# Kernel tuning notes

Measured on AMD Instinct MI355X. Metric: run time of the kernel, lower is better.

Reference implementation:

```python
import jax, jax.numpy as jnp
import numpy as np

N = 2048
IN_C, HID, LAT = 128, 128, 64
E_SPARSE = 65536


def gcn_conv(x, W, b, src, dst, w, n):
    # PyG GCNConv: h = D^-1/2 (A+I) D^-1/2 (x W) + b  (self-loops already in edge list)
    deg = jax.ops.segment_sum(w, dst, num_segments=n)
    dinv = jnp.where(deg > 0, jax.lax.rsqrt(deg), 0.0)
    norm = dinv[src] * w * dinv[dst]            # [E]
    h = x @ W                                   # [N, out]
    agg = jax.ops.segment_sum(h[src] * norm[:, None], dst, num_segments=n)
    return agg + b


def setup_inputs() -> dict:
    key = jax.random.key(0)
    ks = jax.random.split(key, 9)
    x = jax.random.normal(ks[0], (N, IN_C), jnp.float32)
    masked_y = jax.random.normal(ks[1], (N, N), jnp.float32)
    edge_index = jax.random.randint(ks[2], (2, E_SPARSE), 0, N, dtype=jnp.int32)
    s = 0.05
    W1 = jax.random.normal(ks[3], (IN_C, HID), jnp.float32) * s
    b1 = jnp.zeros((HID,), jnp.float32)
    Wmu = jax.random.normal(ks[4], (HID, LAT), jnp.float32) * s
    bmu = jnp.zeros((LAT,), jnp.float32)
    Wls = jax.random.normal(ks[5], (HID, LAT), jnp.float32) * s
    bls = jnp.zeros((LAT,), jnp.float32)
    return {"x": x, "masked_y": masked_y, "W1": W1, "b1": b1,
            "Wmu": Wmu, "bmu": bmu, "Wls": Wls, "bls": bls,
            "edge_index": edge_index}


def reference(x, masked_y, W1, b1, Wmu, bmu, Wls, bls, edge_index):
    n = x.shape[0]
    half = n // 2
    # masking leaves only the top-left [half, half] block of masked_y nonzero;
    # dense_to_sparse on that block -> all half*half (row, col) pairs (entries != 0 a.s.)
    rows = jnp.repeat(jnp.arange(half, dtype=edge_index.dtype), half)
    cols = jnp.tile(jnp.arange(half, dtype=edge_index.dtype), half)
    y_w = jax.nn.sigmoid(masked_y[:half, :half].reshape(-1))
    loop = jnp.arange(n, dtype=edge_index.dtype)
    src = jnp.concatenate([edge_index[0], rows, loop])
    dst = jnp.concatenate([edge_index[1], cols, loop])
    w = jnp.concatenate([jnp.ones((edge_index.shape[1],), x.dtype), y_w,
                         jnp.ones((n,), x.dtype)])
    hidden = jax.nn.relu(gcn_conv(x, W1, b1, src, dst, w, n))
    z_mu = gcn_conv(hidden, Wmu, bmu, src, dst, w, n)
    z_logstd = gcn_conv(hidden, Wls, bls, src, dst, w, n)
    return (z_mu, z_logstd)
```

## Files before the change

### kernel.cpp

```cpp
#include <hip/hip_runtime.h>

#define NN 2048
#define HALF 1024
#define CC 128
#define EE 65536
#define CAP 128

typedef unsigned short u16;

__device__ __forceinline__ float sigm(float v){ return 1.0f/(1.0f + __expf(-v)); }

__device__ __forceinline__ float dinv_lo(int i, const int* __restrict__ cnt,
                                         const float* __restrict__ colsum){
  return rsqrtf(1.0f + (float)cnt[i] + colsum[i]);
}
__device__ __forceinline__ float dinv_any(int i, const int* __restrict__ cnt,
                                          const float* __restrict__ colsum){
  float cs = (i < HALF) ? colsum[i] : 0.0f;
  return rsqrtf(1.0f + (float)cnt[i] + cs);
}

__global__ __launch_bounds__(256) void k_prep(
    const float* __restrict__ my, const int* __restrict__ ei, const float* __restrict__ x,
    const float* __restrict__ W1,
    const float* __restrict__ bmu, const float* __restrict__ bls,
    float* __restrict__ SpRaw, float* __restrict__ colsum,
    int* __restrict__ cnt, u16* __restrict__ bucket, float* __restrict__ H0,
    float* __restrict__ out)
{
  __shared__ float la[8][CC];
  int b = blockIdx.x, t = threadIdx.x;
  int gid = b*256 + t;
  if (gid < 65536) {
    int g4 = (gid & 15)*4;
    const float* bb = (gid < 32768) ? bmu : bls;
    ((float4*)out)[gid] = make_float4(bb[g4], bb[g4+1], bb[g4+2], bb[g4+3]);
  }

  if (b < 128) {
    int c0 = t*4;
    float cs0=0.f, cs1=0.f, cs2=0.f, cs3=0.f;
    #pragma unroll 2
    for (int rr=0; rr<8; ++rr){
      int r = b*8 + rr;
      float4 v = *(const float4*)(my + (size_t)r*NN + c0);
      float s0=sigm(v.x), s1=sigm(v.y), s2=sigm(v.z), s3=sigm(v.w);
      *(float4*)(SpRaw + (size_t)r*HALF + c0) = make_float4(s0,s1,s2,s3);
      cs0+=s0; cs1+=s1; cs2+=s2; cs3+=s3;
    }
    atomicAdd(&colsum[c0+0], cs0);
    atomicAdd(&colsum[c0+1], cs1);
    atomicAdd(&colsum[c0+2], cs2);
    atomicAdd(&colsum[c0+3], cs3);
  } else if (b < 256) {
    int e0 = (b-128)*512 + t;
    #pragma unroll
    for (int i=0;i<2;i++){
      int e = e0 + i*256;
      int s = ei[e], d = ei[EE + e];
      int slot = atomicAdd(&cnt[d], 1);
      if (slot < CAP) bucket[d*CAP + slot] = (u16)s;
    }
  } else {
    int row0 = (b-256)*8;
    #pragma unroll
    for (int i=0;i<4;i++){
      int idx = i*256 + t;
      la[idx>>7][idx&127] = x[(size_t)row0*CC + idx];
    }
    __syncthreads();
    int f = t & 127, rh = t >> 7;
    const float4* a0 = (const float4*)la[rh*4+0];
    const float4* a1 = (const float4*)la[rh*4+1];
    const float4* a2 = (const float4*)la[rh*4+2];
    const float4* a3 = (const float4*)la[rh*4+3];
    float o0=0.f, o1=0.f, o2=0.f, o3=0.f;
    #pragma unroll 4
    for (int k4=0;k4<32;k4++){
      float4 v0=a0[k4], v1=a1[k4], v2=a2[k4], v3=a3[k4];
      float w0 = W1[(k4*4+0)*CC + f];
      float w1 = W1[(k4*4+1)*CC + f];
      float w2 = W1[(k4*4+2)*CC + f];
      float w3 = W1[(k4*4+3)*CC + f];
      o0=fmaf(v0.x,w0,o0); o0=fmaf(v0.y,w1,o0); o0=fmaf(v0.z,w2,o0); o0=fmaf(v0.w,w3,o0);
      o1=fmaf(v1.x,w0,o1); o1=fmaf(v1.y,w1,o1); o1=fmaf(v1.z,w2,o1); o1=fmaf(v1.w,w3,o1);
      o2=fmaf(v2.x,w0,o2); o2=fmaf(v2.y,w1,o2); o2=fmaf(v2.z,w2,o2); o2=fmaf(v2.w,w3,o2);
      o3=fmaf(v3.x,w0,o3); o3=fmaf(v3.y,w1,o3); o3=fmaf(v3.z,w2,o3); o3=fmaf(v3.w,w3,o3);
    }
    H0[(size_t)(row0 + rh*4 + 0)*CC + f] = o0;
    H0[(size_t)(row0 + rh*4 + 1)*CC + f] = o1;
    H0[(size_t)(row0 + rh*4 + 2)*CC + f] = o2;
    H0[(size_t)(row0 + rh*4 + 3)*CC + f] = o3;
  }
}

__global__ __launch_bounds__(256) void k_layer1(
  const float* __restrict__ SpRaw, const float* __restrict__ H0,
  const int* __restrict__ cnt, const float* __restrict__ colsum,
  const u16* __restrict__ bucket,
  float* __restrict__ SP, float* __restrict__ DP)
{
  int b = blockIdx.x, t = threadIdx.x;
  if (b < 512) {
    __shared__ float srow[128];
    int chunk = b & 7, r0 = chunk*128;
    if (t < 128) srow[t] = dinv_lo(r0 + t, cnt, colsum);
    __syncthreads();
    int lane = t & 63, f0 = lane*2;
    int dbase = (b>>3)*16 + (t>>6)*4;
    float a00=0.f,a01=0.f,a10=0.f,a11=0.f,a20=0.f,a21=0.f,a30=0.f,a31=0.f;
    #pragma unroll 4
    for (int rr=0; rr<128; ++rr){
      int r = r0 + rr;
      float2 fv = *(const float2*)(H0 + (size_t)r*CC + f0);
      float sc = srow[rr];
      float fx = fv.x*sc, fy = fv.y*sc;
      float4 s4 = *(const float4*)(SpRaw + (size_t)r*HALF + dbase);
      a00=fmaf(s4.x,fx,a00); a01=fmaf(s4.x,fy,a01);
      a10=fmaf(s4.y,fx,a10); a11=fmaf(s4.y,fy,a11);
      a20=fmaf(s4.z,fx,a20); a21=fmaf(s4.z,fy,a21);
      a30=fmaf(s4.w,fx,a30); a31=fmaf(s4.w,fy,a31);
    }
    float d0=dinv_lo(dbase+0,cnt,colsum), d1=dinv_lo(dbase+1,cnt,colsum);
    float d2=dinv_lo(dbase+2,cnt,colsum), d3=dinv_lo(dbase+3,cnt,colsum);
    float* o = DP + ((size_t)chunk*HALF + dbase)*CC + f0;
    o[0*CC+0]=a00*d0; o[0*CC+1]=a01*d0;
    o[1*CC+0]=a10*d1; o[1*CC+1]=a11*d1;
    o[2*CC+0]=a20*d2; o[2*CC+1]=a21*d2;
    o[3*CC+0]=a30*d3; o[3*CC+1]=a31*d3;
  } else {
    __shared__ float sdinv[NN];
    #pragma unroll
    for (int i=0;i<8;i++){
      int j = i*256 + t;
      float cs = (j < HALF) ? colsum[j] : 0.0f;
      sdinv[j] = rsqrtf(1.0f + (float)cnt[j] + cs);
    }
    __syncthreads();
    int w = t>>6, hw = (t>>5)&1, l = t&31;
    int d = (b-512)*8 + w*2 + hw;
    int f0 = l*4;
    float dd = sdinv[d];
    float4 sv = *(const float4*)(H0 + (size_t)d*CC + f0);
    float ax=dd*sv.x, ay=dd*sv.y, az=dd*sv.z, aw=dd*sv.w;
    int m = cnt[d]; m = m > CAP ? CAP : m;
    const u16* bk = bucket + d*CAP;
    int j = 0;
    for (; j+1 < m; j += 2){
      unsigned pr = *(const unsigned*)(bk + j);
      int s0 = pr & 0xffff, s1 = pr >> 16;
      float w0 = sdinv[s0], w1 = sdinv[s1];
      float4 v0 = *(const float4*)(H0 + (size_t)s0*CC + f0);
      float4 v1 = *(const float4*)(H0 + (size_t)s1*CC + f0);
      ax=fmaf(w0,v0.x,ax); ay=fmaf(w0,v0.y,ay); az=fmaf(w0,v0.z,az); aw=fmaf(w0,v0.w,aw);
      ax=fmaf(w1,v1.x,ax); ay=fmaf(w1,v1.y,ay); az=fmaf(w1,v1.z,az); aw=fmaf(w1,v1.w,aw);
    }
    if (j < m){
      int s0 = bk[j];
      float w0 = sdinv[s0];
      float4 v0 = *(const float4*)(H0 + (size_t)s0*CC + f0);
      ax=fmaf(w0,v0.x,ax); ay=fmaf(w0,v0.y,ay); az=fmaf(w0,v0.z,az); aw=fmaf(w0,v0.w,aw);
    }
    *(float4*)(SP + (size_t)d*CC + f0) = make_float4(dd*ax, dd*ay, dd*az, dd*aw);
  }
}

__global__ __launch_bounds__(256) void k_mid(
  const float* __restrict__ SP, const float* __restrict__ DP,
  const float* __restrict__ b1,
  const float* __restrict__ Wmu, const float* __restrict__ Wls,
  const int* __restrict__ cnt, const float* __restrict__ colsum,
  float* __restrict__ Gm)
{
  __shared__ float la[4][CC];
  int b = blockIdx.x, t = threadIdx.x;
  int row0 = b*4;
  #pragma unroll
  for (int i=0;i<2;i++){
    int idx = i*256 + t;
    int r = row0 + (idx>>7), c = idx & 127;
    float v = SP[(size_t)r*CC + c];
    if (r < HALF){
      #pragma unroll
      for (int k=0;k<8;k++) v += DP[((size_t)k*HALF + r)*CC + c];
    }
    v += b1[c];
    la[idx>>7][c] = v > 0.f ? v : 0.f;
  }
  __syncthreads();
  int f = t & 127, rh = t >> 7, g = f & 63;
  const float* W = (f < 64) ? Wmu : Wls;
  const float4* a0 = (const float4*)la[rh*2+0];
  const float4* a1 = (const float4*)la[rh*2+1];
  float o0=0.f, o1=0.f;
  #pragma unroll 4
  for (int k4=0;k4<32;k4++){
    float4 v0=a0[k4], v1=a1[k4];
    float w0 = W[(k4*4+0)*64 + g];
    float w1 = W[(k4*4+1)*64 + g];
    float w2 = W[(k4*4+2)*64 + g];
    float w3 = W[(k4*4+3)*64 + g];
    o0=fmaf(v0.x,w0,o0); o0=fmaf(v0.y,w1,o0); o0=fmaf(v0.z,w2,o0); o0=fmaf(v0.w,w3,o0);
    o1=fmaf(v1.x,w0,o1); o1=fmaf(v1.y,w1,o1); o1=fmaf(v1.z,w2,o1); o1=fmaf(v1.w,w3,o1);
  }
  int rA = row0 + rh*2;
  Gm[(size_t)(rA+0)*CC + f] = o0 * dinv_any(rA+0, cnt, colsum);
  Gm[(size_t)(rA+1)*CC + f] = o1 * dinv_any(rA+1, cnt, colsum);
}

__global__ __launch_bounds__(256) void k_layer2(
  const float* __restrict__ SpRaw, const float* __restrict__ Gm,
  const int* __restrict__ cnt, const float* __restrict__ colsum,
  const u16* __restrict__ bucket, float* __restrict__ out)
{
  int b = blockIdx.x, t = threadIdx.x;
  if (b < 512) {
    int lane = t & 63, f0 = lane*2;
    size_t obase = (f0 < 64) ? 0 : (size_t)NN*64;
    int g0 = f0 & 63;
    int dbase = (b>>3)*16 + (t>>6)*4;
    int r0 = (b&7)*128;
    float a00=0.f,a01=0.f,a10=0.f,a11=0.f,a20=0.f,a21=0.f,a30=0.f,a31=0.f;
    #pragma unroll 4
    for (int rr=0; rr<128; ++rr){
      int r = r0 + rr;
      float2 gv = *(const float2*)(Gm + (size_t)r*CC + f0);
      float4 s4 = *(const float4*)(SpRaw + (size_t)r*HALF + dbase);
      a00=fmaf(s4.x,gv.x,a00); a01=fmaf(s4.x,gv.y,a01);
      a10=fmaf(s4.y,gv.x,a10); a11=fmaf(s4.y,gv.y,a11);
      a20=fmaf(s4.z,gv.x,a20); a21=fmaf(s4.z,gv.y,a21);
      a30=fmaf(s4.w,gv.x,a30); a31=fmaf(s4.w,gv.y,a31);
    }
    float d0=dinv_lo(dbase+0,cnt,colsum), d1=dinv_lo(dbase+1,cnt,colsum);
    float d2=dinv_lo(dbase+2,cnt,colsum), d3=dinv_lo(dbase+3,cnt,colsum);
    float* o = out + obase + (size_t)dbase*64 + g0;
    atomicAdd(o + 0*64 + 0, a00*d0); atomicAdd(o + 0*64 + 1, a01*d0);
    atomicAdd(o + 1*64 + 0, a10*d1); atomicAdd(o + 1*64 + 1, a11*d1);
    atomicAdd(o + 2*64 + 0, a20*d2); atomicAdd(o + 2*64 + 1, a21*d2);
    atomicAdd(o + 3*64 + 0, a30*d3); atomicAdd(o + 3*64 + 1, a31*d3);
  } else {
    int w = t>>6, hw = (t>>5)&1, l = t&31;
    int d = (b-512)*8 + w*2 + hw;
    int f0 = l*4;
    size_t obase = (f0 < 64) ? 0 : (size_t)NN*64;
    int g0 = f0 & 63;
    float4 a = *(const float4*)(Gm + (size_t)d*CC + f0);
    float ax=a.x, ay=a.y, az=a.z, aw=a.w;
    int m = cnt[d]; m = m > CAP ? CAP : m;
    const u16* bk = bucket + d*CAP;
    int j = 0;
    for (; j+1 < m; j += 2){
      unsigned pr = *(const unsigned*)(bk + j);
      int s0 = pr & 0xffff, s1 = pr >> 16;
      float4 v0 = *(const float4*)(Gm + (size_t)s0*CC + f0);
      float4 v1 = *(const float4*)(Gm + (size_t)s1*CC + f0);
      ax += v0.x + v1.x; ay += v0.y + v1.y;
      az += v0.z + v1.z; aw += v0.w + v1.w;
    }
    if (j < m){
      int s0 = bk[j];
      float4 v0 = *(const float4*)(Gm + (size_t)s0*CC + f0);
      ax += v0.x; ay += v0.y; az += v0.z; aw += v0.w;
    }
    float dd = dinv_any(d, cnt, colsum);
    float* o = out + obase + (size_t)d*64 + g0;
    atomicAdd(o + 0, dd*ax); atomicAdd(o + 1, dd*ay);
    atomicAdd(o + 2, dd*az); atomicAdd(o + 3, dd*aw);
  }
}

extern "C" void kernel_launch(void* const* d_in, const int* in_sizes, int n_in,
                              void* d_out, int out_size, void* d_ws, size_t ws_size,
                              hipStream_t stream)
{
  (void)in_sizes; (void)n_in; (void)out_size; (void)ws_size;
  const float* x   = (const float*)d_in[0];
  const float* my  = (const float*)d_in[1];
  const float* W1  = (const float*)d_in[2];
  const float* b1  = (const float*)d_in[3];
  const float* Wmu = (const float*)d_in[4];
  const float* bmu = (const float*)d_in[5];
  const float* Wls = (const float*)d_in[6];
  const float* bls = (const float*)d_in[7];
  const int*   ei  = (const int*)d_in[8];
  float* out = (float*)d_out;
  char* ws = (char*)d_ws;

  int*   cnt    = (int*)  (ws + 0);
  float* colsum = (float*)(ws + 8192);
  u16*   bucket = (u16*)  (ws + 12288);
  float* SpRaw  = (float*)(ws + 536576);
  float* H0     = (float*)(ws + 4730880);
  float* Gm     = (float*)(ws + 5779456);
  float* SP     = (float*)(ws + 6828032);
  float* DP     = (float*)(ws + 7876608);

  hipMemsetAsync(ws, 0, 12288, stream);
  k_prep  <<<512, 256, 0, stream>>>(my, ei, x, W1, bmu, bls,
                                    SpRaw, colsum, cnt, bucket, H0, out);
  k_layer1<<<768, 256, 0, stream>>>(SpRaw, H0, cnt, colsum, bucket, SP, DP);
  k_mid   <<<512, 256, 0, stream>>>(SP, DP, b1, Wmu, Wls, cnt, colsum, Gm);
  k_layer2<<<768, 256, 0, stream>>>(SpRaw, Gm, cnt, colsum, bucket, out);
}
```

Measured before the change: 153.9 us.

## Aggregate raw x before W1 matmul and widen dense-aggregation register tiles

```diff
diff --git a/kernel.cpp b/kernel.cpp
--- a/kernel.cpp
+++ b/kernel.cpp
@@ -21,22 +21,13 @@
 }
 
 __global__ __launch_bounds__(256) void k_prep(
-    const float* __restrict__ my, const int* __restrict__ ei, const float* __restrict__ x,
-    const float* __restrict__ W1,
+    const float* __restrict__ my, const int* __restrict__ ei,
     const float* __restrict__ bmu, const float* __restrict__ bls,
     float* __restrict__ SpRaw, float* __restrict__ colsum,
-    int* __restrict__ cnt, u16* __restrict__ bucket, float* __restrict__ H0,
+    int* __restrict__ cnt, u16* __restrict__ bucket,
     float* __restrict__ out)
 {
-  __shared__ float la[8][CC];
-  int b = blockIdx.x, t = threadIdx.x;
-  int gid = b*256 + t;
-  if (gid < 65536) {
-    int g4 = (gid & 15)*4;
-    const float* bb = (gid < 32768) ? bmu : bls;
-    ((float4*)out)[gid] = make_float4(bb[g4], bb[g4+1], bb[g4+2], bb[g4+3]);
-  }
-
+  int b = blockIdx.x, t = threadIdx.x;
   if (b < 128) {
     int c0 = t*4;
     float cs0=0.f, cs1=0.f, cs2=0.f, cs3=0.f;
@@ -52,82 +43,54 @@
     atomicAdd(&colsum[c0+1], cs1);
     atomicAdd(&colsum[c0+2], cs2);
     atomicAdd(&colsum[c0+3], cs3);
-  } else if (b < 256) {
-    int e0 = (b-128)*512 + t;
-    #pragma unroll
-    for (int i=0;i<2;i++){
-      int e = e0 + i*256;
-      int s = ei[e], d = ei[EE + e];
-      int slot = atomicAdd(&cnt[d], 1);
-      if (slot < CAP) bucket[d*CAP + slot] = (u16)s;
-    }
   } else {
-    int row0 = (b-256)*8;
-    #pragma unroll
-    for (int i=0;i<4;i++){
-      int idx = i*256 + t;
-      la[idx>>7][idx&127] = x[(size_t)row0*CC + idx];
-    }
-    __syncthreads();
-    int f = t & 127, rh = t >> 7;
-    const float4* a0 = (const float4*)la[rh*4+0];
-    const float4* a1 = (const float4*)la[rh*4+1];
-    const float4* a2 = (const float4*)la[rh*4+2];
-    const float4* a3 = (const float4*)la[rh*4+3];
-    float o0=0.f, o1=0.f, o2=0.f, o3=0.f;
-    #pragma unroll 4
-    for (int k4=0;k4<32;k4++){
-      float4 v0=a0[k4], v1=a1[k4], v2=a2[k4], v3=a3[k4];
-      float w0 = W1[(k4*4+0)*CC + f];
-      float w1 = W1[(k4*4+1)*CC + f];
-      float w2 = W1[(k4*4+2)*CC + f];
-      float w3 = W1[(k4*4+3)*CC + f];
-      o0=fmaf(v0.x,w0,o0); o0=fmaf(v0.y,w1,o0); o0=fmaf(v0.z,w2,o0); o0=fmaf(v0.w,w3,o0);
-      o1=fmaf(v1.x,w0,o1); o1=fmaf(v1.y,w1,o1); o1=fmaf(v1.z,w2,o1); o1=fmaf(v1.w,w3,o1);
-      o2=fmaf(v2.x,w0,o2); o2=fmaf(v2.y,w1,o2); o2=fmaf(v2.z,w2,o2); o2=fmaf(v2.w,w3,o2);
-      o3=fmaf(v3.x,w0,o3); o3=fmaf(v3.y,w1,o3); o3=fmaf(v3.z,w2,o3); o3=fmaf(v3.w,w3,o3);
-    }
-    H0[(size_t)(row0 + rh*4 + 0)*CC + f] = o0;
-    H0[(size_t)(row0 + rh*4 + 1)*CC + f] = o1;
-    H0[(size_t)(row0 + rh*4 + 2)*CC + f] = o2;
-    H0[(size_t)(row0 + rh*4 + 3)*CC + f] = o3;
-  }
-}
-
-__global__ __launch_bounds__(256) void k_layer1(
-  const float* __restrict__ SpRaw, const float* __restrict__ H0,
+    int bb = b - 128;
+    int gid = bb*256 + t;
+    int g4 = (gid & 15)*4;
+    const float* bbias = (gid < 32768) ? bmu : bls;
+    ((float4*)out)[gid] = make_float4(bbias[g4], bbias[g4+1], bbias[g4+2], bbias[g4+3]);
+    int e = bb*256 + t;
+    int s = ei[e], d = ei[EE + e];
+    int slot = atomicAdd(&cnt[d], 1);
+    if (slot < CAP) bucket[d*CAP + slot] = (u16)s;
+  }
+}
+
+__global__ __launch_bounds__(256) void k_agg1(
+  const float* __restrict__ SpRaw, const float* __restrict__ x,
   const int* __restrict__ cnt, const float* __restrict__ colsum,
   const u16* __restrict__ bucket,
   float* __restrict__ SP, float* __restrict__ DP)
 {
   int b = blockIdx.x, t = threadIdx.x;
-  if (b < 512) {
+  if (b < 256) {
     __shared__ float srow[128];
     int chunk = b & 7, r0 = chunk*128;
     if (t < 128) srow[t] = dinv_lo(r0 + t, cnt, colsum);
     __syncthreads();
-    int lane = t & 63, f0 = lane*2;
-    int dbase = (b>>3)*16 + (t>>6)*4;
-    float a00=0.f,a01=0.f,a10=0.f,a11=0.f,a20=0.f,a21=0.f,a30=0.f,a31=0.f;
-    #pragma unroll 4
+    int sub = t >> 5, l = t & 31;
+    int f0 = l*4;
+    int dbase = (b>>3)*32 + sub*4;
+    float4 a0 = make_float4(0.f,0.f,0.f,0.f), a1 = a0, a2 = a0, a3 = a0;
+    #pragma unroll 2
     for (int rr=0; rr<128; ++rr){
       int r = r0 + rr;
-      float2 fv = *(const float2*)(H0 + (size_t)r*CC + f0);
+      float4 xv = *(const float4*)(x + (size_t)r*CC + f0);
       float sc = srow[rr];
-      float fx = fv.x*sc, fy = fv.y*sc;
+      float x0=xv.x*sc, x1=xv.y*sc, x2=xv.z*sc, x3=xv.w*sc;
       float4 s4 = *(const float4*)(SpRaw + (size_t)r*HALF + dbase);
-      a00=fmaf(s4.x,fx,a00); a01=fmaf(s4.x,fy,a01);
-      a10=fmaf(s4.y,fx,a10); a11=fmaf(s4.y,fy,a11);
-      a20=fmaf(s4.z,fx,a20); a21=fmaf(s4.z,fy,a21);
-      a30=fmaf(s4.w,fx,a30); a31=fmaf(s4.w,fy,a31);
+      a0.x=fmaf(s4.x,x0,a0.x); a0.y=fmaf(s4.x,x1,a0.y); a0.z=fmaf(s4.x,x2,a0.z); a0.w=fmaf(s4.x,x3,a0.w);
+      a1.x=fmaf(s4.y,x0,a1.x); a1.y=fmaf(s4.y,x1,a1.y); a1.z=fmaf(s4.y,x2,a1.z); a1.w=fmaf(s4.y,x3,a1.w);
+      a2.x=fmaf(s4.z,x0,a2.x); a2.y=fmaf(s4.z,x1,a2.y); a2.z=fmaf(s4.z,x2,a2.z); a2.w=fmaf(s4.z,x3,a2.w);
+      a3.x=fmaf(s4.w,x0,a3.x); a3.y=fmaf(s4.w,x1,a3.y); a3.z=fmaf(s4.w,x2,a3.z); a3.w=fmaf(s4.w,x3,a3.w);
     }
     float d0=dinv_lo(dbase+0,cnt,colsum), d1=dinv_lo(dbase+1,cnt,colsum);
     float d2=dinv_lo(dbase+2,cnt,colsum), d3=dinv_lo(dbase+3,cnt,colsum);
     float* o = DP + ((size_t)chunk*HALF + dbase)*CC + f0;
-    o[0*CC+0]=a00*d0; o[0*CC+1]=a01*d0;
-    o[1*CC+0]=a10*d1; o[1*CC+1]=a11*d1;
-    o[2*CC+0]=a20*d2; o[2*CC+1]=a21*d2;
-    o[3*CC+0]=a30*d3; o[3*CC+1]=a31*d3;
+    *(float4*)(o + 0*CC) = make_float4(a0.x*d0, a0.y*d0, a0.z*d0, a0.w*d0);
+    *(float4*)(o + 1*CC) = make_float4(a1.x*d1, a1.y*d1, a1.z*d1, a1.w*d1);
+    *(float4*)(o + 2*CC) = make_float4(a2.x*d2, a2.y*d2, a2.z*d2, a2.w*d2);
+    *(float4*)(o + 3*CC) = make_float4(a3.x*d3, a3.y*d3, a3.z*d3, a3.w*d3);
   } else {
     __shared__ float sdinv[NN];
     #pragma unroll
@@ -138,10 +101,10 @@
     }
     __syncthreads();
     int w = t>>6, hw = (t>>5)&1, l = t&31;
-    int d = (b-512)*8 + w*2 + hw;
+    int d = (b-256)*8 + w*2 + hw;
     int f0 = l*4;
     float dd = sdinv[d];
-    float4 sv = *(const float4*)(H0 + (size_t)d*CC + f0);
+    float4 sv = *(const float4*)(x + (size_t)d*CC + f0);
     float ax=dd*sv.x, ay=dd*sv.y, az=dd*sv.z, aw=dd*sv.w;
     int m = cnt[d]; m = m > CAP ? CAP : m;
     const u16* bk = bucket + d*CAP;
@@ -150,15 +113,15 @@
       unsigned pr = *(const unsigned*)(bk + j);
       int s0 = pr & 0xffff, s1 = pr >> 16;
       float w0 = sdinv[s0], w1 = sdinv[s1];
-      float4 v0 = *(const float4*)(H0 + (size_t)s0*CC + f0);
-      float4 v1 = *(const float4*)(H0 + (size_t)s1*CC + f0);
+      float4 v0 = *(const float4*)(x + (size_t)s0*CC + f0);
+      float4 v1 = *(const float4*)(x + (size_t)s1*CC + f0);
       ax=fmaf(w0,v0.x,ax); ay=fmaf(w0,v0.y,ay); az=fmaf(w0,v0.z,az); aw=fmaf(w0,v0.w,aw);
       ax=fmaf(w1,v1.x,ax); ay=fmaf(w1,v1.y,ay); az=fmaf(w1,v1.z,az); aw=fmaf(w1,v1.w,aw);
     }
     if (j < m){
       int s0 = bk[j];
       float w0 = sdinv[s0];
-      float4 v0 = *(const float4*)(H0 + (size_t)s0*CC + f0);
+      float4 v0 = *(const float4*)(x + (size_t)s0*CC + f0);
       ax=fmaf(w0,v0.x,ax); ay=fmaf(w0,v0.y,ay); az=fmaf(w0,v0.z,az); aw=fmaf(w0,v0.w,aw);
     }
     *(float4*)(SP + (size_t)d*CC + f0) = make_float4(dd*ax, dd*ay, dd*az, dd*aw);
@@ -167,12 +130,13 @@
 
 __global__ __launch_bounds__(256) void k_mid(
   const float* __restrict__ SP, const float* __restrict__ DP,
-  const float* __restrict__ b1,
+  const float* __restrict__ b1, const float* __restrict__ W1,
   const float* __restrict__ Wmu, const float* __restrict__ Wls,
   const int* __restrict__ cnt, const float* __restrict__ colsum,
   float* __restrict__ Gm)
 {
   __shared__ float la[4][CC];
+  __shared__ float lb[4][CC];
   int b = blockIdx.x, t = threadIdx.x;
   int row0 = b*4;
   #pragma unroll
@@ -184,63 +148,90 @@
       #pragma unroll
       for (int k=0;k<8;k++) v += DP[((size_t)k*HALF + r)*CC + c];
     }
-    v += b1[c];
-    la[idx>>7][c] = v > 0.f ? v : 0.f;
+    la[idx>>7][c] = v;
   }
   __syncthreads();
-  int f = t & 127, rh = t >> 7, g = f & 63;
-  const float* W = (f < 64) ? Wmu : Wls;
-  const float4* a0 = (const float4*)la[rh*2+0];
-  const float4* a1 = (const float4*)la[rh*2+1];
-  float o0=0.f, o1=0.f;
-  #pragma unroll 4
-  for (int k4=0;k4<32;k4++){
-    float4 v0=a0[k4], v1=a1[k4];
-    float w0 = W[(k4*4+0)*64 + g];
-    float w1 = W[(k4*4+1)*64 + g];
-    float w2 = W[(k4*4+2)*64 + g];
-    float w3 = W[(k4*4+3)*64 + g];
-    o0=fmaf(v0.x,w0,o0); o0=fmaf(v0.y,w1,o0); o0=fmaf(v0.z,w2,o0); o0=fmaf(v0.w,w3,o0);
-    o1=fmaf(v1.x,w0,o1); o1=fmaf(v1.y,w1,o1); o1=fmaf(v1.z,w2,o1); o1=fmaf(v1.w,w3,o1);
-  }
-  int rA = row0 + rh*2;
-  Gm[(size_t)(rA+0)*CC + f] = o0 * dinv_any(rA+0, cnt, colsum);
-  Gm[(size_t)(rA+1)*CC + f] = o1 * dinv_any(rA+1, cnt, colsum);
-}
-
-__global__ __launch_bounds__(256) void k_layer2(
+  int f = t & 127, rh = t >> 7;
+  {
+    const float4* a0 = (const float4*)la[rh*2+0];
+    const float4* a1 = (const float4*)la[rh*2+1];
+    float o0=0.f, o1=0.f;
+    #pragma unroll 4
+    for (int k4=0;k4<32;k4++){
+      float4 v0=a0[k4], v1=a1[k4];
+      float w0 = W1[(k4*4+0)*CC + f];
+      float w1 = W1[(k4*4+1)*CC + f];
+      float w2 = W1[(k4*4+2)*CC + f];
+      float w3 = W1[(k4*4+3)*CC + f];
+      o0=fmaf(v0.x,w0,o0); o0=fmaf(v0.y,w1,o0); o0=fmaf(v0.z,w2,o0); o0=fmaf(v0.w,w3,o0);
+      o1=fmaf(v1.x,w0,o1); o1=fmaf(v1.y,w1,o1); o1=fmaf(v1.z,w2,o1); o1=fmaf(v1.w,w3,o1);
+    }
+    float bb = b1[f];
+    o0 += bb; o1 += bb;
+    lb[rh*2+0][f] = o0 > 0.f ? o0 : 0.f;
+    lb[rh*2+1][f] = o1 > 0.f ? o1 : 0.f;
+  }
+  __syncthreads();
+  {
+    int g = f & 63;
+    const float* W = (f < 64) ? Wmu : Wls;
+    const float4* a0 = (const float4*)lb[rh*2+0];
+    const float4* a1 = (const float4*)lb[rh*2+1];
+    float o0=0.f, o1=0.f;
+    #pragma unroll 4
+    for (int k4=0;k4<32;k4++){
+      float4 v0=a0[k4], v1=a1[k4];
+      float w0 = W[(k4*4+0)*64 + g];
+      float w1 = W[(k4*4+1)*64 + g];
+      float w2 = W[(k4*4+2)*64 + g];
+      float w3 = W[(k4*4+3)*64 + g];
+      o0=fmaf(v0.x,w0,o0); o0=fmaf(v0.y,w1,o0); o0=fmaf(v0.z,w2,o0); o0=fmaf(v0.w,w3,o0);
+      o1=fmaf(v1.x,w0,o1); o1=fmaf(v1.y,w1,o1); o1=fmaf(v1.z,w2,o1); o1=fmaf(v1.w,w3,o1);
+    }
+    int rA = row0 + rh*2;
+    Gm[(size_t)(rA+0)*CC + f] = o0 * dinv_any(rA+0, cnt, colsum);
+    Gm[(size_t)(rA+1)*CC + f] = o1 * dinv_any(rA+1, cnt, colsum);
+  }
+}
+
+__global__ __launch_bounds__(256) void k_agg2(
   const float* __restrict__ SpRaw, const float* __restrict__ Gm,
   const int* __restrict__ cnt, const float* __restrict__ colsum,
   const u16* __restrict__ bucket, float* __restrict__ out)
 {
   int b = blockIdx.x, t = threadIdx.x;
-  if (b < 512) {
-    int lane = t & 63, f0 = lane*2;
+  if (b < 128) {
+    int sub = t >> 5, l = t & 31;
+    int f0 = l*4;
+    int dbase = (b>>2)*32 + sub*4;
+    int r0 = (b&3)*256;
+    float4 a0 = make_float4(0.f,0.f,0.f,0.f), a1 = a0, a2 = a0, a3 = a0;
+    #pragma unroll 2
+    for (int rr=0; rr<256; ++rr){
+      int r = r0 + rr;
+      float4 gv = *(const float4*)(Gm + (size_t)r*CC + f0);
+      float4 s4 = *(const float4*)(SpRaw + (size_t)r*HALF + dbase);
+      a0.x=fmaf(s4.x,gv.x,a0.x); a0.y=fmaf(s4.x,gv.y,a0.y); a0.z=fmaf(s4.x,gv.z,a0.z); a0.w=fmaf(s4.x,gv.w,a0.w);
+      a1.x=fmaf(s4.y,gv.x,a1.x); a1.y=fmaf(s4.y,gv.y,a1.y); a1.z=fmaf(s4.y,gv.z,a1.z); a1.w=fmaf(s4.y,gv.w,a1.w);
+      a2.x=fmaf(s4.z,gv.x,a2.x); a2.y=fmaf(s4.z,gv.y,a2.y); a2.z=fmaf(s4.z,gv.z,a2.z); a2.w=fmaf(s4.z,gv.w,a2.w);
+      a3.x=fmaf(s4.w,gv.x,a3.x); a3.y=fmaf(s4.w,gv.y,a3.y); a3.z=fmaf(s4.w,gv.z,a3.z); a3.w=fmaf(s4.w,gv.w,a3.w);
+    }
     size_t obase = (f0 < 64) ? 0 : (size_t)NN*64;
     int g0 = f0 & 63;
-    int dbase = (b>>3)*16 + (t>>6)*4;
-    int r0 = (b&7)*128;
-    float a00=0.f,a01=0.f,a10=0.f,a11=0.f,a20=0.f,a21=0.f,a30=0.f,a31=0.f;
-    #pragma unroll 4
-    for (int rr=0; rr<128; ++rr){
-      int r = r0 + rr;
-      float2 gv = *(const float2*)(Gm + (size_t)r*CC + f0);
-      float4 s4 = *(const float4*)(SpRaw + (size_t)r*HALF + dbase);
-      a00=fmaf(s4.x,gv.x,a00); a01=fmaf(s4.x,gv.y,a01);
-      a10=fmaf(s4.y,gv.x,a10); a11=fmaf(s4.y,gv.y,a11);
-      a20=fmaf(s4.z,gv.x,a20); a21=fmaf(s4.z,gv.y,a21);
-      a30=fmaf(s4.w,gv.x,a30); a31=fmaf(s4.w,gv.y,a31);
-    }
     float d0=dinv_lo(dbase+0,cnt,colsum), d1=dinv_lo(dbase+1,cnt,colsum);
     float d2=dinv_lo(dbase+2,cnt,colsum), d3=dinv_lo(dbase+3,cnt,colsum);
     float* o = out + obase + (size_t)dbase*64 + g0;
-    atomicAdd(o + 0*64 + 0, a00*d0); atomicAdd(o + 0*64 + 1, a01*d0);
-    atomicAdd(o + 1*64 + 0, a10*d1); atomicAdd(o + 1*64 + 1, a11*d1);
-    atomicAdd(o + 2*64 + 0, a20*d2); atomicAdd(o + 2*64 + 1, a21*d2);
-    atomicAdd(o + 3*64 + 0, a30*d3); atomicAdd(o + 3*64 + 1, a31*d3);
+    atomicAdd(o + 0*64 + 0, a0.x*d0); atomicAdd(o + 0*64 + 1, a0.y*d0);
+    atomicAdd(o + 0*64 + 2, a0.z*d0); atomicAdd(o + 0*64 + 3, a0.w*d0);
+    atomicAdd(o + 1*64 + 0, a1.x*d1); atomicAdd(o + 1*64 + 1, a1.y*d1);
+    atomicAdd(o + 1*64 + 2, a1.z*d1); atomicAdd(o + 1*64 + 3, a1.w*d1);
+    atomicAdd(o + 2*64 + 0, a2.x*d2); atomicAdd(o + 2*64 + 1, a2.y*d2);
+    atomicAdd(o + 2*64 + 2, a2.z*d2); atomicAdd(o + 2*64 + 3, a2.w*d2);
+    atomicAdd(o + 3*64 + 0, a3.x*d3); atomicAdd(o + 3*64 + 1, a3.y*d3);
+    atomicAdd(o + 3*64 + 2, a3.z*d3); atomicAdd(o + 3*64 + 3, a3.w*d3);
   } else {
     int w = t>>6, hw = (t>>5)&1, l = t&31;
-    int d = (b-512)*8 + w*2 + hw;
+    int d = (b-128)*8 + w*2 + hw;
     int f0 = l*4;
     size_t obase = (f0 < 64) ? 0 : (size_t)NN*64;
     int g0 = f0 & 63;
@@ -290,15 +281,13 @@
   float* colsum = (float*)(ws + 8192);
   u16*   bucket = (u16*)  (ws + 12288);
   float* SpRaw  = (float*)(ws + 536576);
-  float* H0     = (float*)(ws + 4730880);
-  float* Gm     = (float*)(ws + 5779456);
-  float* SP     = (float*)(ws + 6828032);
-  float* DP     = (float*)(ws + 7876608);
+  float* Gm     = (float*)(ws + 4730880);
+  float* SP     = (float*)(ws + 5779456);
+  float* DP     = (float*)(ws + 6828032);
 
   hipMemsetAsync(ws, 0, 12288, stream);
-  k_prep  <<<512, 256, 0, stream>>>(my, ei, x, W1, bmu, bls,
-                                    SpRaw, colsum, cnt, bucket, H0, out);
-  k_layer1<<<768, 256, 0, stream>>>(SpRaw, H0, cnt, colsum, bucket, SP, DP);
-  k_mid   <<<512, 256, 0, stream>>>(SP, DP, b1, Wmu, Wls, cnt, colsum, Gm);
-  k_layer2<<<768, 256, 0, stream>>>(SpRaw, Gm, cnt, colsum, bucket, out);
-}
+  k_prep<<<384, 256, 0, stream>>>(my, ei, bmu, bls, SpRaw, colsum, cnt, bucket, out);
+  k_agg1<<<512, 256, 0, stream>>>(SpRaw, x, cnt, colsum, bucket, SP, DP);
+  k_mid <<<512, 256, 0, stream>>>(SP, DP, b1, W1, Wmu, Wls, cnt, colsum, Gm);
+  k_agg2<<<384, 256, 0, stream>>>(SpRaw, Gm, cnt, colsum, bucket, out);
+}
```

After: 186.3 us. 1.21x slower.
